# Optimization experiments

Measured on AMD Instinct MI355X. Metric: run time of the kernel, lower is better.

## Reference

```python
import jax, jax.numpy as jnp
import numpy as np
from jax.scipy.special import logsumexp

N = 20000      # nodes
E = 320000     # input (undirected) edges
F_IN = 128
HID = 128
C = 8          # num_classes
ITERS = 100


def setup_inputs() -> dict:
    key = jax.random.key(0)
    ks = jax.random.split(key, 10)
    x = jax.random.normal(ks[0], (N, F_IN), dtype=jnp.float32)
    edge_index = jax.random.randint(ks[1], (2, E), 0, N)
    train_mask = jax.random.randint(ks[2], (N,), 0, 2).astype(bool)
    target = jax.random.randint(ks[3], (N,), 0, C)
    W1 = jax.random.normal(ks[4], (F_IN, HID), dtype=jnp.float32) / np.sqrt(F_IN).astype(np.float32)
    b1 = jnp.zeros((HID,), jnp.float32)
    W2 = jax.random.normal(ks[5], (HID, C), dtype=jnp.float32) / np.sqrt(HID).astype(np.float32)
    b2 = jnp.zeros((C,), jnp.float32)
    binary = (jax.random.normal(ks[6], (C, C), dtype=jnp.float32) + jnp.eye(C, dtype=jnp.float32)) / C
    rezero = 0.1 * jax.random.normal(ks[7], (E,), dtype=jnp.float32)
    return dict(x=x, edge_index=edge_index, train_mask=train_mask, target=target,
                W1=W1, b1=b1, W2=W2, b2=b2, binary=binary, rezero=rezero)


def _forward(x, edge_index, train_mask, target, W1, b1, W2, b2, binary, rezero):
    n = x.shape[0]
    # pairwise_edge_idx: make both directions of every edge (directed edge list, Ed = 2E)
    s0, d0 = edge_index[0], edge_index[1]
    src = jnp.concatenate([s0, d0])
    dst = jnp.concatenate([d0, s0])
    Ed = src.shape[0]

    # ---- GCN backbone (eval mode -> no dropout). GCNConv: sym-norm A-hat with self loops.
    sl = jnp.arange(n)
    gsrc = jnp.concatenate([src, sl])
    gdst = jnp.concatenate([dst, sl])
    degs = jax.ops.segment_sum(jnp.ones((gsrc.shape[0],), x.dtype), gdst, num_segments=n)
    dinv = jax.lax.rsqrt(jnp.maximum(degs, 1.0))
    enorm = dinv[gsrc] * dinv[gdst]  # [Ed+n]

    def conv(h, W, b):
        h = h @ W
        msg = h[gsrc] * enorm[:, None]
        return jax.ops.segment_sum(msg, gdst, num_segments=n) + b

    h = jax.nn.relu(conv(x, W1, b1))
    unary = conv(h, W2, b2)                       # [N, C]
    B = (binary + binary.T) / 2                   # symmetrized pairwise potential

    # ---- loopy_bp preprocessing (energies, GT clamping) -- torch.no_grad in original
    e_un = -unary
    gt_vals = jnp.take_along_axis(e_un, target[:, None], axis=1)  # GT energies, gathered first
    oh = jax.nn.one_hot(target, C, dtype=bool)
    e_un = jnp.where(train_mask[:, None], 1e5, e_un)
    e_un = jnp.where(train_mask[:, None] & oh, gt_vals, e_un)
    e_un = e_un - e_un.min(axis=1, keepdims=True)
    e_bin = -B
    e_bin = e_bin - e_bin.min()
    e_un = jnp.minimum(e_un, 20.0)
    phi_u = jax.lax.stop_gradient(-e_un)          # log node potentials
    phi_b = jax.lax.stop_gradient(-e_bin)         # log pairwise potential [C, C]
    scales = jax.lax.stop_gradient(jnp.concatenate([rezero, rezero]))  # per directed edge

    # reverse-edge index: edge i's reverse is i+E (mod 2E) by construction
    rev = (jnp.arange(Ed) + Ed // 2) % Ed

    def step(m, _):
        node_in = jax.ops.segment_sum(m, dst, num_segments=n)       # [N, C] sum of incoming msgs
        hmsg = (phi_u + node_in)[src] - m[rev]                       # [Ed, C] exclude reverse msg
        t = hmsg[:, :, None] + scales[:, None, None] * phi_b[None]   # [Ed, C, C]
        m_new = logsumexp(t, axis=1)                                 # marginalize sender label
        m_new = m_new - logsumexp(m_new, axis=1, keepdims=True)      # renormalize per iteration
        return m_new, None

    m0 = jnp.zeros((Ed, C), phi_u.dtype)
    m, _ = jax.lax.scan(step, m0, None, length=ITERS)

    beliefs = phi_u + jax.ops.segment_sum(m, dst, num_segments=n)
    return jax.nn.log_softmax(beliefs, axis=1)    # node_logits


def reference(x, edge_index, train_mask, target, W1, b1, W2, b2, binary, rezero):
    return _forward(x, edge_index, train_mask, target, W1, b1, W2, b2, binary, rezero)
```

## Files before the change

kernel.cpp:

```cpp
#include <hip/hip_runtime.h>
#include <hip/hip_bf16.h>

#define NN 20000
#define EU 320000
#define ED 640000
#define FIN 128
#define HD  128
#define NC  8
#define BP_ITERS 100
#define NPB 4
#define GMAX 16

#define LOG2E 1.4426950408889634f
#define LN2   0.6931471805599453f

enum {
  OFF_FLAG   = 0,
  OFF_DINV   = 4,
  OFF_COUNT  = OFF_DINV  + NN,
  OFF_ROWPTR = OFF_COUNT + NN,
  OFF_FILL   = OFF_ROWPTR+ NN + 4,
  OFF_EID    = OFF_FILL  + NN,
  OFF_POS    = OFF_EID   + ED,
  OFF_SRC    = OFF_POS   + ED,
  OFF_REV    = OFF_SRC   + ED,
  OFF_SCALE  = OFF_REV   + ED,
  OFF_HW2    = OFF_SCALE + ED,
  OFF_PHIU   = OFF_HW2   + NN*NC,
  OFF_PHIB   = OFF_PHIU  + NN*NC,
  OFF_MA     = OFF_PHIB  + 64,
  OFF_MB     = OFF_MA    + ED*NC,
  WS_WORDS   = OFF_MB    + ED*NC
};

__device__ __forceinline__ float fexp2(float x) {
#if __has_builtin(__builtin_amdgcn_exp2f)
  return __builtin_amdgcn_exp2f(x);
#else
  return exp2f(x);
#endif
}
__device__ __forceinline__ float flog2(float x) {
#if __has_builtin(__builtin_amdgcn_logf)
  return __builtin_amdgcn_logf(x);
#else
  return log2f(x);
#endif
}

__global__ void k_detect(const unsigned* tm, int* flag) {
  __shared__ int bad;
  if (threadIdx.x == 0) bad = 0;
  __syncthreads();
  for (int i = threadIdx.x; i < NN / 4; i += blockDim.x) {
    if (tm[i] > 1u) atomicOr(&bad, 1);
  }
  __syncthreads();
  if (threadIdx.x == 0) flag[0] = bad;
}

__global__ void k_count(const int* ei, int* cnt) {
  int e = blockIdx.x * blockDim.x + threadIdx.x;
  if (e < ED) {
    int er = (e < EU) ? e + EU : e - EU;
    atomicAdd(&cnt[ei[er]], 1);
  }
}

__global__ void k_scan(const int* cnt, int* rowptr) {
  __shared__ int s[1024];
  const int T = 1024, CH = (NN + T - 1) / T;
  int t = threadIdx.x;
  int base = t * CH;
  int loc = 0;
  for (int k = 0; k < CH; k++) {
    int idx = base + k;
    if (idx < NN) loc += cnt[idx];
  }
  s[t] = loc;
  __syncthreads();
  for (int off = 1; off < T; off <<= 1) {
    int v = (t >= off) ? s[t - off] : 0;
    __syncthreads();
    s[t] += v;
    __syncthreads();
  }
  int run = s[t] - loc;
  for (int k = 0; k < CH; k++) {
    int idx = base + k;
    if (idx < NN) { rowptr[idx] = run; run += cnt[idx]; }
  }
  if (t == T - 1) rowptr[NN] = run;
}

__global__ void k_dinv(const int* cnt, float* dinv) {
  int v = blockIdx.x * blockDim.x + threadIdx.x;
  if (v < NN) dinv[v] = rsqrtf((float)(cnt[v] + 1));
}

__global__ void k_fill(const int* ei, const int* rowptr, int* fill,
                       int* eid, int* pos, int* srcarr, float* scale_s,
                       const float* rezero) {
  int e = blockIdx.x * blockDim.x + threadIdx.x;
  if (e < ED) {
    int er = (e < EU) ? e + EU : e - EU;
    int dst = ei[er];
    int p = rowptr[dst] + atomicAdd(&fill[dst], 1);
    eid[p] = e;
    pos[e] = p;
    srcarr[p] = ei[e];
    scale_s[p] = rezero[(e < EU) ? e : e - EU];
  }
}

__global__ void k_rev(const int* eid, const int* pos, int* revslot) {
  int p = blockIdx.x * blockDim.x + threadIdx.x;
  if (p < ED) {
    int e = eid[p];
    int er = (e < EU) ? e + EU : e - EU;
    revslot[p] = pos[er];
  }
}

__global__ __launch_bounds__(256) void k_gemm1(const float* __restrict__ x,
                                               const float* __restrict__ W1,
                                               const float* __restrict__ dinv,
                                               float* __restrict__ hw1) {
  int t = threadIdx.x;
  int c = t & 127, half = t >> 7;
  int r0 = blockIdx.x * 32 + half * 16;
  float acc[16];
#pragma unroll
  for (int r = 0; r < 16; r++) acc[r] = 0.f;
  for (int k = 0; k < FIN; k++) {
    float w = W1[k * HD + c];
#pragma unroll
    for (int r = 0; r < 16; r++)
      acc[r] += x[(r0 + r) * FIN + k] * w;
  }
#pragma unroll
  for (int r = 0; r < 16; r++)
    hw1[(r0 + r) * HD + c] = acc[r] * dinv[r0 + r];
}

__global__ __launch_bounds__(128) void k_agg1(const float* __restrict__ hw1,
                                              const float* __restrict__ dinv,
                                              const int* __restrict__ rowptr,
                                              const int* __restrict__ srcarr,
                                              const float* __restrict__ b1,
                                              float* __restrict__ h1) {
  int v = blockIdx.x;
  int f = threadIdx.x;
  int s0 = rowptr[v], s1 = rowptr[v + 1];
  float a0 = 0.f, a1 = 0.f, a2 = 0.f, a3 = 0.f;
  int s = s0;
  for (; s + 4 <= s1; s += 4) {
    int u0 = srcarr[s], u1 = srcarr[s + 1], u2 = srcarr[s + 2], u3 = srcarr[s + 3];
    a0 += hw1[u0 * HD + f];
    a1 += hw1[u1 * HD + f];
    a2 += hw1[u2 * HD + f];
    a3 += hw1[u3 * HD + f];
  }
  for (; s < s1; s++) a0 += hw1[srcarr[s] * HD + f];
  float acc = (a0 + a1) + (a2 + a3);
  float dv = dinv[v];
  float val = dv * (acc + hw1[v * HD + f]) + b1[f];
  h1[v * HD + f] = fmaxf(val, 0.f);
}

__global__ __launch_bounds__(256) void k_gemm2(const float* __restrict__ h1,
                                               const float* __restrict__ W2,
                                               const float* __restrict__ dinv,
                                               float* __restrict__ hw2) {
  __shared__ float Ws[HD * NC];
  int t = threadIdx.x;
  for (int i = t; i < HD * NC; i += 256) Ws[i] = W2[i];
  __syncthreads();
  int v = blockIdx.x * 256 + t;
  if (v >= NN) return;
  float acc[NC];
#pragma unroll
  for (int c = 0; c < NC; c++) acc[c] = 0.f;
  const float4* hp = (const float4*)&h1[v * HD];
  for (int k4 = 0; k4 < HD / 4; k4++) {
    float4 h4 = hp[k4];
    float hv[4] = {h4.x, h4.y, h4.z, h4.w};
#pragma unroll
    for (int j = 0; j < 4; j++) {
      int k = k4 * 4 + j;
#pragma unroll
      for (int c = 0; c < NC; c++) acc[c] += hv[j] * Ws[k * NC + c];
    }
  }
  float dv = dinv[v];
#pragma unroll
  for (int c = 0; c < NC; c++) hw2[v * NC + c] = acc[c] * dv;
}

__global__ __launch_bounds__(256) void k_agg2pre(const float* __restrict__ hw2,
                                                 const float* __restrict__ dinv,
                                                 const int* __restrict__ rowptr,
                                                 const int* __restrict__ srcarr,
                                                 const float* __restrict__ b2,
                                                 const int* __restrict__ target,
                                                 const void* __restrict__ tmask,
                                                 const int* __restrict__ flag,
                                                 float* __restrict__ phi_u) {
  int t = threadIdx.x;
  int node = blockIdx.x * 32 + (t >> 3);
  int c = t & 7;
  if (node >= NN) return;
  int s0 = rowptr[node], s1 = rowptr[node + 1];
  float acc = 0.f;
  for (int s = s0; s < s1; s++) {
    int u = srcarr[s];
    acc += hw2[u * NC + c];
  }
  float dv = dinv[node];
  float unary = dv * (acc + hw2[node * NC + c]) + b2[c];
  float e = -unary;
  int tgt = target[node];
  float gt = __shfl(e, (t & ~7) | tgt, 64);
  bool mk;
  if (flag[0]) mk = ((const unsigned char*)tmask)[node] != 0;
  else         mk = ((const int*)tmask)[node] != 0;
  if (mk) e = (c == tgt) ? gt : 1e5f;
  float mn = e;
  mn = fminf(mn, __shfl_xor(mn, 1));
  mn = fminf(mn, __shfl_xor(mn, 2));
  mn = fminf(mn, __shfl_xor(mn, 4));
  e = fminf(e - mn, 20.0f);
  phi_u[node * NC + c] = -e;
}

__global__ void k_phib(const float* __restrict__ binary, float* __restrict__ phib) {
  int t = threadIdx.x;
  int i = t >> 3, j = t & 7;
  float B = 0.5f * (binary[i * NC + j] + binary[j * NC + i]);
  float mx = B;
#pragma unroll
  for (int d = 1; d < 64; d <<= 1) mx = fmaxf(mx, __shfl_xor(mx, d));
  phib[t] = B - mx;
}

__global__ __launch_bounds__(256) void k_bp(const float* __restrict__ m,
                                            float* __restrict__ mout,
                                            const float* __restrict__ phiu,
                                            const int* __restrict__ rowptr,
                                            const int* __restrict__ revslot,
                                            const float* __restrict__ scale_s,
                                            const float* __restrict__ phib_g) {
  __shared__ float pb[64];
  int t = threadIdx.x;
  if (t < 64) pb[t] = phib_g[t];
  __syncthreads();
  int w = t >> 6, l = t & 63, le = l >> 3, c = l & 7;
  int v = blockIdx.x * NPB + w;
  int s0 = rowptr[v], deg = rowptr[v + 1] - s0;
  int ng = (deg + 7) >> 3;
  float pbr[8];
#pragma unroll
  for (int i = 0; i < 8; i++) pbr[i] = pb[i * 8 + c];

  float mv[GMAX];
  float ni = 0.f;
#pragma unroll
  for (int g = 0; g < GMAX; g++) {
    mv[g] = 0.f;
    if (g < ng) {
      int q = g * 8 + le;
      if (q < deg) mv[g] = m[(s0 + q) * 8 + c];
      ni += mv[g];
    }
  }
  for (int g = GMAX; g < ng; g++) {
    int q = g * 8 + le;
    if (q < deg) ni += m[(s0 + q) * 8 + c];
  }
  ni += __shfl_xor(ni, 8);
  ni += __shfl_xor(ni, 16);
  ni += __shfl_xor(ni, 32);
  float nph = phiu[v * 8 + c] + ni;

#pragma unroll
  for (int g = 0; g < GMAX; g++) {
    if (g < ng) {
      int q = g * 8 + le;
      float hm = nph - mv[g];
      float mx = hm;
      mx = fmaxf(mx, __shfl_xor(mx, 1));
      mx = fmaxf(mx, __shfl_xor(mx, 2));
      mx = fmaxf(mx, __shfl_xor(mx, 4));
      float a = (hm - mx) * LOG2E;
      float sl = scale_s[s0 + (q < deg ? q : 0)] * LOG2E;
      float S = 0.f;
#pragma unroll
      for (int i = 0; i < 8; i++) {
        float ai = __shfl(a, (l & 56) | i, 64);
        S += fexp2(fmaf(sl, pbr[i], ai));
      }
      float out = fmaf(flog2(S), LN2, mx);
      float mm = out;
      mm = fmaxf(mm, __shfl_xor(mm, 1));
      mm = fmaxf(mm, __shfl_xor(mm, 2));
      mm = fmaxf(mm, __shfl_xor(mm, 4));
      float Z = fexp2((out - mm) * LOG2E);
      Z += __shfl_xor(Z, 1);
      Z += __shfl_xor(Z, 2);
      Z += __shfl_xor(Z, 4);
      float res = out - fmaf(flog2(Z), LN2, mm);
      if (q < deg) mout[revslot[s0 + q] * 8 + c] = res;
    }
  }
  for (int g = GMAX; g < ng; g++) {
    int q = g * 8 + le;
    float mvg = (q < deg) ? m[(s0 + q) * 8 + c] : 0.f;
    float hm = nph - mvg;
    float mx = hm;
    mx = fmaxf(mx, __shfl_xor(mx, 1));
    mx = fmaxf(mx, __shfl_xor(mx, 2));
    mx = fmaxf(mx, __shfl_xor(mx, 4));
    float a = (hm - mx) * LOG2E;
    float sl = scale_s[s0 + (q < deg ? q : 0)] * LOG2E;
    float S = 0.f;
#pragma unroll
    for (int i = 0; i < 8; i++) {
      float ai = __shfl(a, (l & 56) | i, 64);
      S += fexp2(fmaf(sl, pbr[i], ai));
    }
    float out = fmaf(flog2(S), LN2, mx);
    float mm = out;
    mm = fmaxf(mm, __shfl_xor(mm, 1));
    mm = fmaxf(mm, __shfl_xor(mm, 2));
    mm = fmaxf(mm, __shfl_xor(mm, 4));
    float Z = fexp2((out - mm) * LOG2E);
    Z += __shfl_xor(Z, 1);
    Z += __shfl_xor(Z, 2);
    Z += __shfl_xor(Z, 4);
    float res = out - fmaf(flog2(Z), LN2, mm);
    if (q < deg) mout[revslot[s0 + q] * 8 + c] = res;
  }
}

__global__ __launch_bounds__(256) void k_final(const float* __restrict__ m,
                                               const float* __restrict__ phiu,
                                               const int* __restrict__ rowptr,
                                               float* __restrict__ out) {
  int t = threadIdx.x;
  int w = t >> 6, l = t & 63, le = l >> 3, c = l & 7;
  int v = blockIdx.x * NPB + w;
  int s0 = rowptr[v], deg = rowptr[v + 1] - s0;
  float ni = 0.f;
  for (int q = le; q < deg; q += 8) ni += m[(s0 + q) * 8 + c];
  ni += __shfl_xor(ni, 8);
  ni += __shfl_xor(ni, 16);
  ni += __shfl_xor(ni, 32);
  float bel = phiu[v * 8 + c] + ni;
  float mx = bel;
  mx = fmaxf(mx, __shfl_xor(mx, 1));
  mx = fmaxf(mx, __shfl_xor(mx, 2));
  mx = fmaxf(mx, __shfl_xor(mx, 4));
  float Z = fexp2((bel - mx) * LOG2E);
  Z += __shfl_xor(Z, 1);
  Z += __shfl_xor(Z, 2);
  Z += __shfl_xor(Z, 4);
  out[v * 8 + c] = bel - fmaf(flog2(Z), LN2, mx);
}

extern "C" void kernel_launch(void* const* d_in, const int* in_sizes, int n_in,
                              void* d_out, int out_size, void* d_ws, size_t ws_size,
                              hipStream_t stream) {
  const float* x      = (const float*)d_in[0];
  const int*   ei     = (const int*)d_in[1];
  const void*  tmask  = d_in[2];
  const int*   target = (const int*)d_in[3];
  const float* W1     = (const float*)d_in[4];
  const float* b1     = (const float*)d_in[5];
  const float* W2     = (const float*)d_in[6];
  const float* b2     = (const float*)d_in[7];
  const float* binary = (const float*)d_in[8];
  const float* rezero = (const float*)d_in[9];

  float* ws  = (float*)d_ws;
  int*   wsi = (int*)d_ws;

  int*   flag    = wsi + OFF_FLAG;
  float* dinv    = ws  + OFF_DINV;
  int*   cnt     = wsi + OFF_COUNT;
  int*   rowptr  = wsi + OFF_ROWPTR;
  int*   fill    = wsi + OFF_FILL;
  int*   eid     = wsi + OFF_EID;
  int*   pos     = wsi + OFF_POS;
  int*   srcarr  = wsi + OFF_SRC;
  int*   revslot = wsi + OFF_REV;
  float* scale_s = ws  + OFF_SCALE;
  float* hw2     = ws  + OFF_HW2;
  float* phiu    = ws  + OFF_PHIU;
  float* phib    = ws  + OFF_PHIB;
  float* mA      = ws  + OFF_MA;
  float* mB      = ws  + OFF_MB;
  float* hw1     = mA;
  float* h1      = mB;

  hipMemsetAsync(cnt, 0, NN * sizeof(int), stream);
  hipMemsetAsync(fill, 0, NN * sizeof(int), stream);

  k_detect<<<1, 1024, 0, stream>>>((const unsigned*)tmask, flag);
  k_count<<<(ED + 255) / 256, 256, 0, stream>>>(ei, cnt);
  k_scan<<<1, 1024, 0, stream>>>(cnt, rowptr);
  k_dinv<<<(NN + 255) / 256, 256, 0, stream>>>(cnt, dinv);
  k_fill<<<(ED + 255) / 256, 256, 0, stream>>>(ei, rowptr, fill, eid, pos,
                                               srcarr, scale_s, rezero);
  k_rev<<<(ED + 255) / 256, 256, 0, stream>>>(eid, pos, revslot);

  k_gemm1<<<NN / 32, 256, 0, stream>>>(x, W1, dinv, hw1);
  k_agg1<<<NN, 128, 0, stream>>>(hw1, dinv, rowptr, srcarr, b1, h1);
  k_gemm2<<<(NN + 255) / 256, 256, 0, stream>>>(h1, W2, dinv, hw2);
  k_agg2pre<<<NN / 32, 256, 0, stream>>>(hw2, dinv, rowptr, srcarr, b2, target,
                                         tmask, flag, phiu);
  k_phib<<<1, 64, 0, stream>>>(binary, phib);

  hipMemsetAsync(mA, 0, (size_t)ED * NC * sizeof(float), stream);

  float* mcur = mA;
  float* mnxt = mB;
  for (int it = 0; it < BP_ITERS; it++) {
    k_bp<<<NN / NPB, 256, 0, stream>>>(mcur, mnxt, phiu, rowptr, revslot,
                                       scale_s, phib);
    float* tmp = mcur; mcur = mnxt; mnxt = tmp;
  }

  k_final<<<NN / NPB, 256, 0, stream>>>(mcur, phiu, rowptr, (float*)d_out);
}
```

Measured before the change: 2.971 ms.

## Split BP step into per-node sum and per-edge thread kernels

Replaces the fused per-node belief propagation kernel, where one wavefront handles a node and uses lane shuffles for the 8x8 logsumexp, with two kernels. A node kernel writes the summed incoming messages plus unary into a new nphi buffer, and an edge kernel gives each directed edge its own thread with vectorized float4 loads and in-register reductions. The aim is to remove the load imbalance from uneven degrees, the shuffle overhead and the register-cached message array. The cost is a second launch per iteration, an extra read of the messages and nphi, and scattered nphi gathers. The first GEMM is also retiled to 8 rows per thread with float4 loads of x.

```diff
diff --git a/kernel.cpp b/kernel.cpp
--- a/kernel.cpp
+++ b/kernel.cpp
@@ -9,7 +9,6 @@
 #define NC  8
 #define BP_ITERS 100
 #define NPB 4
-#define GMAX 16
 
 #define LOG2E 1.4426950408889634f
 #define LN2   0.6931471805599453f
@@ -28,7 +27,8 @@
   OFF_HW2    = OFF_SCALE + ED,
   OFF_PHIU   = OFF_HW2   + NN*NC,
   OFF_PHIB   = OFF_PHIU  + NN*NC,
-  OFF_MA     = OFF_PHIB  + 64,
+  OFF_NPHI   = OFF_PHIB  + 64,
+  OFF_MA     = OFF_NPHI  + NN*NC,
   OFF_MB     = OFF_MA    + ED*NC,
   WS_WORDS   = OFF_MB    + ED*NC
 };
@@ -113,12 +113,13 @@
   }
 }
 
-__global__ void k_rev(const int* eid, const int* pos, int* revslot) {
+__global__ void k_rev(int* eid, const int* pos, int* revslot, const int* ei) {
   int p = blockIdx.x * blockDim.x + threadIdx.x;
   if (p < ED) {
     int e = eid[p];
     int er = (e < EU) ? e + EU : e - EU;
     revslot[p] = pos[er];
+    eid[p] = ei[er];
   }
 }
 
@@ -128,18 +129,23 @@
                                                float* __restrict__ hw1) {
   int t = threadIdx.x;
   int c = t & 127, half = t >> 7;
-  int r0 = blockIdx.x * 32 + half * 16;
-  float acc[16];
-#pragma unroll
-  for (int r = 0; r < 16; r++) acc[r] = 0.f;
-  for (int k = 0; k < FIN; k++) {
-    float w = W1[k * HD + c];
-#pragma unroll
-    for (int r = 0; r < 16; r++)
-      acc[r] += x[(r0 + r) * FIN + k] * w;
-  }
-#pragma unroll
-  for (int r = 0; r < 16; r++)
+  int r0 = blockIdx.x * 16 + half * 8;
+  float acc[8];
+#pragma unroll
+  for (int r = 0; r < 8; r++) acc[r] = 0.f;
+  for (int k = 0; k < FIN; k += 4) {
+    float w0 = W1[k * HD + c];
+    float w1 = W1[(k + 1) * HD + c];
+    float w2 = W1[(k + 2) * HD + c];
+    float w3 = W1[(k + 3) * HD + c];
+#pragma unroll
+    for (int r = 0; r < 8; r++) {
+      float4 xr = *(const float4*)&x[(r0 + r) * FIN + k];
+      acc[r] += xr.x * w0 + xr.y * w1 + xr.z * w2 + xr.w * w3;
+    }
+  }
+#pragma unroll
+  for (int r = 0; r < 8; r++)
     hw1[(r0 + r) * HD + c] = acc[r] * dinv[r0 + r];
 }
 
@@ -243,103 +249,65 @@
   phib[t] = B - mx;
 }
 
-__global__ __launch_bounds__(256) void k_bp(const float* __restrict__ m,
-                                            float* __restrict__ mout,
-                                            const float* __restrict__ phiu,
-                                            const int* __restrict__ rowptr,
-                                            const int* __restrict__ revslot,
-                                            const float* __restrict__ scale_s,
-                                            const float* __restrict__ phib_g) {
-  __shared__ float pb[64];
-  int t = threadIdx.x;
-  if (t < 64) pb[t] = phib_g[t];
-  __syncthreads();
+__global__ __launch_bounds__(256) void k_node(const float* __restrict__ m,
+                                              const float* __restrict__ phiu,
+                                              const int* __restrict__ rowptr,
+                                              float* __restrict__ nphi) {
+  int t = threadIdx.x;
   int w = t >> 6, l = t & 63, le = l >> 3, c = l & 7;
   int v = blockIdx.x * NPB + w;
   int s0 = rowptr[v], deg = rowptr[v + 1] - s0;
-  int ng = (deg + 7) >> 3;
-  float pbr[8];
-#pragma unroll
-  for (int i = 0; i < 8; i++) pbr[i] = pb[i * 8 + c];
-
-  float mv[GMAX];
   float ni = 0.f;
-#pragma unroll
-  for (int g = 0; g < GMAX; g++) {
-    mv[g] = 0.f;
-    if (g < ng) {
-      int q = g * 8 + le;
-      if (q < deg) mv[g] = m[(s0 + q) * 8 + c];
-      ni += mv[g];
-    }
-  }
-  for (int g = GMAX; g < ng; g++) {
-    int q = g * 8 + le;
-    if (q < deg) ni += m[(s0 + q) * 8 + c];
-  }
+  for (int q = le; q < deg; q += 8) ni += m[(s0 + q) * 8 + c];
   ni += __shfl_xor(ni, 8);
   ni += __shfl_xor(ni, 16);
   ni += __shfl_xor(ni, 32);
-  float nph = phiu[v * 8 + c] + ni;
-
-#pragma unroll
-  for (int g = 0; g < GMAX; g++) {
-    if (g < ng) {
-      int q = g * 8 + le;
-      float hm = nph - mv[g];
-      float mx = hm;
-      mx = fmaxf(mx, __shfl_xor(mx, 1));
-      mx = fmaxf(mx, __shfl_xor(mx, 2));
-      mx = fmaxf(mx, __shfl_xor(mx, 4));
-      float a = (hm - mx) * LOG2E;
-      float sl = scale_s[s0 + (q < deg ? q : 0)] * LOG2E;
-      float S = 0.f;
-#pragma unroll
-      for (int i = 0; i < 8; i++) {
-        float ai = __shfl(a, (l & 56) | i, 64);
-        S += fexp2(fmaf(sl, pbr[i], ai));
-      }
-      float out = fmaf(flog2(S), LN2, mx);
-      float mm = out;
-      mm = fmaxf(mm, __shfl_xor(mm, 1));
-      mm = fmaxf(mm, __shfl_xor(mm, 2));
-      mm = fmaxf(mm, __shfl_xor(mm, 4));
-      float Z = fexp2((out - mm) * LOG2E);
-      Z += __shfl_xor(Z, 1);
-      Z += __shfl_xor(Z, 2);
-      Z += __shfl_xor(Z, 4);
-      float res = out - fmaf(flog2(Z), LN2, mm);
-      if (q < deg) mout[revslot[s0 + q] * 8 + c] = res;
-    }
-  }
-  for (int g = GMAX; g < ng; g++) {
-    int q = g * 8 + le;
-    float mvg = (q < deg) ? m[(s0 + q) * 8 + c] : 0.f;
-    float hm = nph - mvg;
-    float mx = hm;
-    mx = fmaxf(mx, __shfl_xor(mx, 1));
-    mx = fmaxf(mx, __shfl_xor(mx, 2));
-    mx = fmaxf(mx, __shfl_xor(mx, 4));
-    float a = (hm - mx) * LOG2E;
-    float sl = scale_s[s0 + (q < deg ? q : 0)] * LOG2E;
+  if (le == 0) nphi[v * 8 + c] = phiu[v * 8 + c] + ni;
+}
+
+__global__ __launch_bounds__(256) void k_edge(const float* __restrict__ m,
+                                              float* __restrict__ mout,
+                                              const float* __restrict__ nphi,
+                                              const int* __restrict__ dstof,
+                                              const int* __restrict__ revslot,
+                                              const float* __restrict__ scale_s,
+                                              const float* __restrict__ phib_g) {
+  int p = blockIdx.x * 256 + threadIdx.x;
+  int v = dstof[p];
+  float4 m0 = *(const float4*)&m[p * 8];
+  float4 m1 = *(const float4*)&m[p * 8 + 4];
+  float4 n0 = *(const float4*)&nphi[v * 8];
+  float4 n1 = *(const float4*)&nphi[v * 8 + 4];
+  float hm[8] = {n0.x - m0.x, n0.y - m0.y, n0.z - m0.z, n0.w - m0.w,
+                 n1.x - m1.x, n1.y - m1.y, n1.z - m1.z, n1.w - m1.w};
+  float mx = hm[0];
+#pragma unroll
+  for (int i = 1; i < 8; i++) mx = fmaxf(mx, hm[i]);
+  float a[8];
+#pragma unroll
+  for (int i = 0; i < 8; i++) a[i] = (hm[i] - mx) * LOG2E;
+  float sl = scale_s[p] * LOG2E;
+  float out[8];
+#pragma unroll
+  for (int j = 0; j < 8; j++) {
     float S = 0.f;
 #pragma unroll
-    for (int i = 0; i < 8; i++) {
-      float ai = __shfl(a, (l & 56) | i, 64);
-      S += fexp2(fmaf(sl, pbr[i], ai));
-    }
-    float out = fmaf(flog2(S), LN2, mx);
-    float mm = out;
-    mm = fmaxf(mm, __shfl_xor(mm, 1));
-    mm = fmaxf(mm, __shfl_xor(mm, 2));
-    mm = fmaxf(mm, __shfl_xor(mm, 4));
-    float Z = fexp2((out - mm) * LOG2E);
-    Z += __shfl_xor(Z, 1);
-    Z += __shfl_xor(Z, 2);
-    Z += __shfl_xor(Z, 4);
-    float res = out - fmaf(flog2(Z), LN2, mm);
-    if (q < deg) mout[revslot[s0 + q] * 8 + c] = res;
-  }
+    for (int i = 0; i < 8; i++)
+      S += fexp2(fmaf(sl, phib_g[i * 8 + j], a[i]));
+    out[j] = fmaf(flog2(S), LN2, mx);
+  }
+  float mm = out[0];
+#pragma unroll
+  for (int j = 1; j < 8; j++) mm = fmaxf(mm, out[j]);
+  float Z = 0.f;
+#pragma unroll
+  for (int j = 0; j < 8; j++) Z += fexp2((out[j] - mm) * LOG2E);
+  float lse = fmaf(flog2(Z), LN2, mm);
+  int rp = revslot[p];
+  float4 o0 = make_float4(out[0] - lse, out[1] - lse, out[2] - lse, out[3] - lse);
+  float4 o1 = make_float4(out[4] - lse, out[5] - lse, out[6] - lse, out[7] - lse);
+  *(float4*)&mout[rp * 8] = o0;
+  *(float4*)&mout[rp * 8 + 4] = o1;
 }
 
 __global__ __launch_bounds__(256) void k_final(const float* __restrict__ m,
@@ -397,6 +365,7 @@
   float* hw2     = ws  + OFF_HW2;
   float* phiu    = ws  + OFF_PHIU;
   float* phib    = ws  + OFF_PHIB;
+  float* nphi    = ws  + OFF_NPHI;
   float* mA      = ws  + OFF_MA;
   float* mB      = ws  + OFF_MB;
   float* hw1     = mA;
@@ -411,9 +380,9 @@
   k_dinv<<<(NN + 255) / 256, 256, 0, stream>>>(cnt, dinv);
   k_fill<<<(ED + 255) / 256, 256, 0, stream>>>(ei, rowptr, fill, eid, pos,
                                                srcarr, scale_s, rezero);
-  k_rev<<<(ED + 255) / 256, 256, 0, stream>>>(eid, pos, revslot);
-
-  k_gemm1<<<NN / 32, 256, 0, stream>>>(x, W1, dinv, hw1);
+  k_rev<<<(ED + 255) / 256, 256, 0, stream>>>(eid, pos, revslot, ei);
+
+  k_gemm1<<<NN / 16, 256, 0, stream>>>(x, W1, dinv, hw1);
   k_agg1<<<NN, 128, 0, stream>>>(hw1, dinv, rowptr, srcarr, b1, h1);
   k_gemm2<<<(NN + 255) / 256, 256, 0, stream>>>(h1, W2, dinv, hw2);
   k_agg2pre<<<NN / 32, 256, 0, stream>>>(hw2, dinv, rowptr, srcarr, b2, target,
@@ -425,8 +394,9 @@
   float* mcur = mA;
   float* mnxt = mB;
   for (int it = 0; it < BP_ITERS; it++) {
-    k_bp<<<NN / NPB, 256, 0, stream>>>(mcur, mnxt, phiu, rowptr, revslot,
-                                       scale_s, phib);
+    k_node<<<NN / NPB, 256, 0, stream>>>(mcur, phiu, rowptr, nphi);
+    k_edge<<<ED / 256, 256, 0, stream>>>(mcur, mnxt, nphi, eid, revslot,
+                                         scale_s, phib);
     float* tmp = mcur; mcur = mnxt; mnxt = tmp;
   }
 
```

Measured after the change: 2.561 ms. -13.8%, faster.
